# Kernel tuning notes

Measured on AMD Instinct MI355X. Metric: run time of the kernel, lower is better.

Reference implementation:

```python
import jax, jax.numpy as jnp
import numpy as np

NMS_THR = 0.7
TOPK = 128      # fixed post-NMS rois per level (static padding for jit)
OUT = 14        # RoIAlign output size
SAMPLES = 2     # samples per bin per dim (fixed approximation of sampling_ratio=-1)
STRIDES = (32.0, 16.0, 8.0)


def get_channel(a):
    # a: [..., 4] boxes as (cx, cy, w, h); FPN level assignment, clamped to [1, 4]
    s = jnp.sqrt(a[..., 2] * a[..., 3])
    return jnp.clip(jnp.floor(3.0 + jnp.log2(s / 224.0)), 1.0, 4.0)


def cxcywh_to_xyxy(b):
    cx, cy, w, h = b[..., 0], b[..., 1], b[..., 2], b[..., 3]
    return jnp.stack([cx - w / 2, cy - h / 2, cx + w / 2, cy + h / 2], axis=-1)


def pairwise_iou(b):
    x1, y1, x2, y2 = b[:, 0], b[:, 1], b[:, 2], b[:, 3]
    area = jnp.maximum(x2 - x1, 0.0) * jnp.maximum(y2 - y1, 0.0)
    ix1 = jnp.maximum(x1[:, None], x1[None, :])
    iy1 = jnp.maximum(y1[:, None], y1[None, :])
    ix2 = jnp.minimum(x2[:, None], x2[None, :])
    iy2 = jnp.minimum(y2[:, None], y2[None, :])
    inter = jnp.maximum(ix2 - ix1, 0.0) * jnp.maximum(iy2 - iy1, 0.0)
    union = area[:, None] + area[None, :] - inter
    return inter / jnp.maximum(union, 1e-9)


def nms_keep(boxes_xyxy, scores, thr):
    # Greedy NMS over masked scores (-inf entries sort last and are excluded later).
    n = scores.shape[0]
    order = jnp.argsort(-scores)
    iou = pairwise_iou(boxes_xyxy[order])  # [N, N]
    idx = jnp.arange(n)

    def body(sup, i):
        keep_i = ~sup[i]
        sup = sup | (keep_i & (iou[i] > thr) & (idx > i))
        return sup, keep_i

    _, keeps_sorted = jax.lax.scan(body, jnp.zeros(n, dtype=bool), idx)
    return jnp.zeros(n, dtype=bool).at[order].set(keeps_sorted)


def roi_align(feat, boxes):
    # feat: [C, H, W]; boxes: [K, 4]. NOTE: the original prepare_boxes feeds
    # (cx, cy, w, h) straight into RoIAlign, which interprets them as
    # (x1, y1, x2, y2) -- replicated faithfully here. spatial_scale = 1.
    C, H, W = feat.shape
    K = boxes.shape[0]
    x1, y1, x2, y2 = boxes[:, 0], boxes[:, 1], boxes[:, 2], boxes[:, 3]
    rw = jnp.maximum(x2 - x1, 1.0)
    rh = jnp.maximum(y2 - y1, 1.0)
    bw = rw / OUT
    bh = rh / OUT
    # fractional bin offsets, [OUT*SAMPLES]
    f = (jnp.arange(OUT, dtype=feat.dtype)[:, None]
         + (jnp.arange(SAMPLES, dtype=feat.dtype)[None, :] + 0.5) / SAMPLES).reshape(-1)
    ys = y1[:, None] + bh[:, None] * f[None, :]  # [K, S]
    xs = x1[:, None] + bw[:, None] * f[None, :]
    Y = ys[:, :, None]  # [K, S, 1]
    X = xs[:, None, :]  # [K, 1, S]
    valid = (Y > -1.0) & (Y < H) & (X > -1.0) & (X < W)  # [K, S, S]
    Yc = jnp.clip(Y, 0.0, H - 1.0)
    Xc = jnp.clip(X, 0.0, W - 1.0)
    y0 = jnp.floor(Yc)
    x0 = jnp.floor(Xc)
    y0i = y0.astype(jnp.int32)
    x0i = x0.astype(jnp.int32)
    y1i = jnp.minimum(y0i + 1, H - 1)
    x1i = jnp.minimum(x0i + 1, W - 1)
    ly = Yc - y0
    lx = Xc - x0
    hy = 1.0 - ly
    hx = 1.0 - lx
    g = lambda yi, xi: feat[:, yi, xi]  # -> [C, K, S, S]
    val = (g(y0i, x0i) * (hy * hx) + g(y0i, x1i) * (hy * lx)
           + g(y1i, x0i) * (ly * hx) + g(y1i, x1i) * (ly * lx))
    val = val * valid.astype(val.dtype)
    val = val.reshape(C, K, OUT, SAMPLES, OUT, SAMPLES).mean(axis=(3, 5))
    return jnp.transpose(val, (1, 0, 2, 3))  # [K, C, OUT, OUT]


def level_extract(feat, boxes, scores, levs, nl):
    # one image, one target FPN level: mask, NMS, fixed top-K select, RoIAlign
    mask = levs == nl
    msc = jnp.where(mask, scores, -jnp.inf)
    xyxy = cxcywh_to_xyxy(boxes)
    keep = nms_keep(jax.lax.stop_gradient(xyxy), jax.lax.stop_gradient(msc), NMS_THR)
    eff = jnp.where(keep & mask, msc, -jnp.inf)
    vals, sel = jax.lax.top_k(jax.lax.stop_gradient(eff), TOPK)
    valid = jnp.isfinite(vals)
    rois = boxes[sel] * valid[:, None].astype(boxes.dtype)
    out = roi_align(feat, rois)
    return out * valid[:, None, None, None].astype(out.dtype)


def _forward(p32, p16, p8, p4, a32, a16, a8, s32, s16, s8):
    anchors = (a32, a16, a8)  # p4 proposals are computed then discarded in the
    # original (grouping loop only runs l in range(3)); p4 features are never
    # RoIAligned either (nl loops 1..3), so p4 only appears as an unused input.
    levs = jnp.concatenate([get_channel(a) for a in anchors], axis=1)      # [B, N]
    boxes = jnp.concatenate([a * s for a, s in zip(anchors, STRIDES)], axis=1)
    scores = jnp.concatenate([s32, s16, s8], axis=1)
    outs = []
    for nl, feat in zip((1.0, 2.0, 3.0), (p32, p16, p8)):
        fn = jax.vmap(lambda f, b, s, l, nl=nl: level_extract(f, b, s, l, nl))
        outs.append(fn(feat, boxes, scores, levs))  # [B, TOPK, C, 14, 14]
    return jnp.concatenate(outs, axis=1)  # [B, 3*TOPK, C, 14, 14]


def setup_inputs():
    key = jax.random.key(0)
    ks = jax.random.split(key, 10)
    B, C = 2, 256
    p32 = jax.random.normal(ks[0], (B, C, 32, 32), jnp.float32)
    p16 = jax.random.normal(ks[1], (B, C, 64, 64), jnp.float32)
    p8 = jax.random.normal(ks[2], (B, C, 128, 128), jnp.float32)
    p4 = jax.random.normal(ks[3], (B, C, 256, 256), jnp.float32)

    def mk_anchors(k, n, hf):
        k1, k2 = jax.random.split(k)
        cxy = jax.random.uniform(k1, (B, n, 2), jnp.float32) * hf
        wh = 16.0 + jax.random.uniform(k2, (B, n, 2), jnp.float32) * 434.0
        return jnp.concatenate([cxy, wh], axis=-1)

    anchors_32 = mk_anchors(ks[4], 512, 32.0)
    anchors_16 = mk_anchors(ks[5], 1024, 64.0)
    anchors_8 = mk_anchors(ks[6], 2048, 128.0)
    scores_32 = jax.random.normal(ks[7], (B, 512), jnp.float32)
    scores_16 = jax.random.normal(ks[8], (B, 1024), jnp.float32)
    scores_8 = jax.random.normal(ks[9], (B, 2048), jnp.float32)
    return dict(p32=p32, p16=p16, p8=p8, p4=p4,
                anchors_32=anchors_32, anchors_16=anchors_16, anchors_8=anchors_8,
                scores_32=scores_32, scores_16=scores_16, scores_8=scores_8)


def reference(p32, p16, p8, p4, anchors_32, anchors_16, anchors_8,
              scores_32, scores_16, scores_8):
    return _forward(p32, p16, p8, p4, anchors_32, anchors_16, anchors_8,
                    scores_32, scores_16, scores_8)
```

## Files before the change

kernel.cpp:

```cpp
#include <hip/hip_runtime.h>
#include <stdint.h>

#define NMS_THR 0.7f
#define TOPK 128
#define NTOT 3584
#define NROW 4096
#define NW 64
#define OUTSZ 14
#define NSAMP 28

typedef unsigned long long u64;
typedef float vf4 __attribute__((ext_vector_type(4)));

__device__ __forceinline__ void fetch_anchor(
    const float* __restrict__ a32, const float* __restrict__ a16,
    const float* __restrict__ a8,
    const float* __restrict__ s32, const float* __restrict__ s16,
    const float* __restrict__ s8,
    int b, int i, float* A, float* st, float* sc)
{
    const float* P;
    if (i < 512) {
        P = a32 + (b * 512 + i) * 4;  *st = 32.0f; *sc = s32[b * 512 + i];
    } else if (i < 1536) {
        int j = i - 512;
        P = a16 + (b * 1024 + j) * 4; *st = 16.0f; *sc = s16[b * 1024 + j];
    } else {
        int j = i - 1536;
        P = a8 + (b * 2048 + j) * 4;  *st = 8.0f;  *sc = s8[b * 2048 + j];
    }
    A[0] = P[0]; A[1] = P[1]; A[2] = P[2]; A[3] = P[3];
}

__global__ __launch_bounds__(1024) void sortprep_kernel(
    const float* __restrict__ a32, const float* __restrict__ a16,
    const float* __restrict__ a8,
    const float* __restrict__ s32, const float* __restrict__ s16,
    const float* __restrict__ s8,
    float* __restrict__ sbox,
    float* __restrict__ scbox,
    int* __restrict__ mArr)
{
    __shared__ u64 key[NROW];
    __shared__ int mCount;
    int prob = blockIdx.x;
    int b = prob / 3;
    int nl = prob % 3 + 1;
    int tid = threadIdx.x;

    if (tid == 0) mCount = 0;
    __syncthreads();

    for (int i = tid; i < NTOT; i += 1024) {
        float A[4], st, sc;
        fetch_anchor(a32, a16, a8, s32, s16, s8, b, i, A, &st, &sc);
        float s = sqrtf(__fmul_rn(A[2], A[3]));
        float lv = floorf(__fadd_rn(3.0f, log2f(__fdiv_rn(s, 224.0f))));
        lv = fminf(fmaxf(lv, 1.0f), 4.0f);
        if ((int)lv == nl) {
            unsigned u = __float_as_uint(sc);
            u = (u & 0x80000000u) ? ~u : (u | 0x80000000u);
            unsigned d = ~u;
            int pos = atomicAdd(&mCount, 1);
            key[pos] = ((u64)d << 32) | (unsigned)i;
        }
    }
    __syncthreads();
    int m = mCount;
    int P2 = 64;
    while (P2 < m) P2 <<= 1;
    for (int i = m + tid; i < P2; i += 1024) key[i] = ~0ull;
    __syncthreads();

    for (int k = 2; k <= P2; k <<= 1) {
        for (int j = k >> 1; j > 0; j >>= 1) {
            for (int t = tid; t < P2; t += 1024) {
                int ixj = t ^ j;
                if (ixj > t) {
                    u64 a = key[t], bb = key[ixj];
                    bool up = ((t & k) == 0);
                    if ((a > bb) == up) { key[t] = bb; key[ixj] = a; }
                }
            }
            __syncthreads();
        }
    }

    for (int r = tid; r < m; r += 1024) {
        int orig = (int)(key[r] & 0xffffffffu);
        float A[4], st, sc;
        fetch_anchor(a32, a16, a8, s32, s16, s8, b, orig, A, &st, &sc);
        float cx = A[0] * st, cy = A[1] * st, w = A[2] * st, h = A[3] * st;
        float4 cw = make_float4(cx, cy, w, h);
        float4 v;
        v.x = __fsub_rn(cx, 0.5f * w);
        v.y = __fsub_rn(cy, 0.5f * h);
        v.z = __fadd_rn(cx, 0.5f * w);
        v.w = __fadd_rn(cy, 0.5f * h);
        ((float4*)(sbox + (size_t)prob * NROW * 4))[r] = v;
        ((float4*)(scbox + (size_t)prob * NROW * 4))[r] = cw;
    }
    if (tid == 0) mArr[prob] = m;
}

__global__ __launch_bounds__(256) void mask_kernel(
    const float* __restrict__ sbox, const int* __restrict__ mArr,
    u64* __restrict__ mask)
{
    int prob = blockIdx.x >> 10;
    int rgrp = blockIdx.x & 1023;
    int wave = threadIdx.x >> 6;
    int lane = threadIdx.x & 63;
    int row = rgrp * 4 + wave;
    int m = mArr[prob];
    if (row >= m) return;

    const float4* SB = (const float4*)(sbox + (size_t)prob * NROW * 4);
    float4 bi = SB[row];
    float areai = __fmul_rn(fmaxf(__fsub_rn(bi.z, bi.x), 0.0f),
                            fmaxf(__fsub_rn(bi.w, bi.y), 0.0f));
    u64* outm = mask + ((size_t)prob * NROW + row) * NW;
    int cEnd = (m - 1) >> 6;
    for (int c = row >> 6; c <= cEnd; c++) {
        int col = c * 64 + lane;
        bool p = false;
        if (col < m) {
            float4 bj = SB[col];
            float areaj = __fmul_rn(fmaxf(__fsub_rn(bj.z, bj.x), 0.0f),
                                    fmaxf(__fsub_rn(bj.w, bj.y), 0.0f));
            float ix1 = fmaxf(bi.x, bj.x);
            float iy1 = fmaxf(bi.y, bj.y);
            float ix2 = fminf(bi.z, bj.z);
            float iy2 = fminf(bi.w, bj.w);
            float inter = __fmul_rn(fmaxf(__fsub_rn(ix2, ix1), 0.0f),
                                    fmaxf(__fsub_rn(iy2, iy1), 0.0f));
            float uni = __fsub_rn(__fadd_rn(areai, areaj), inter);
            float iou = __fdiv_rn(inter, fmaxf(uni, 1e-9f));
            p = iou > NMS_THR;
        }
        u64 bal = __ballot(p);
        if (lane == 0) outm[c] = bal;
    }
}

__global__ __launch_bounds__(64) void scan_kernel(
    const float* __restrict__ scbox, const int* __restrict__ mArr,
    const u64* __restrict__ mask,
    float* __restrict__ rois,
    int* __restrict__ validOut)
{
    __shared__ int selList[TOPK];
    int prob = blockIdx.x;
    int lane = threadIdx.x;
    int m = mArr[prob];
    const u64* M = mask + (size_t)prob * NROW * NW;

    u64 sup;
    if (lane * 64 >= m) sup = ~0ull;
    else if (lane * 64 + 64 > m) sup = ~0ull << (m & 63);
    else sup = 0ull;

    int kept = 0;
    int cur = 0;
    while (kept < TOPK && cur < m) {
        int cw = cur >> 6;
        u64 validm = (lane < cw) ? 0ull : (lane == cw ? (~0ull << (cur & 63)) : ~0ull);
        u64 avail = ~sup & validm;
        u64 bal = __ballot(avail != 0ull);
        if (bal == 0ull) break;
        int fl = __builtin_ctzll(bal);
        int lo = __shfl((int)(unsigned)avail, fl);
        int hi = __shfl((int)(avail >> 32), fl);
        u64 w = ((u64)(unsigned)hi << 32) | (unsigned)lo;
        int j = fl * 64 + __builtin_ctzll(w);

        if (lane == 0) selList[kept] = j;
        kept++;
        if (lane >= (j >> 6)) sup |= M[(size_t)j * NW + lane];
        cur = j + 1;
    }
    __syncthreads();

    for (int k = lane; k < TOPK; k += 64) {
        float4 rv = make_float4(0.0f, 0.0f, 0.0f, 0.0f);
        int vld = 0;
        if (k < kept) {
            rv = ((const float4*)(scbox + (size_t)prob * NROW * 4))[selList[k]];
            vld = 1;
        }
        ((float4*)(rois + ((size_t)prob * TOPK + k) * 4))[0] = rv;
        validOut[prob * TOPK + k] = vld;
    }
}

__global__ __launch_bounds__(256) void repack_kernel(
    const float* __restrict__ p32, const float* __restrict__ p16,
    const float* __restrict__ p8,
    float* __restrict__ ft0, float* __restrict__ ft1, float* __restrict__ ft2)
{
    __shared__ float tile[64][65];
    int id = blockIdx.x;
    const float* F; float* T; int HW, b, t;
    if (id < 128)       { F = p32; T = ft0; HW = 1024;  b = id / 64;  t = id % 64; }
    else if (id < 640)  { id -= 128; F = p16; T = ft1; HW = 4096;  b = id / 256; t = id % 256; }
    else                { id -= 640; F = p8;  T = ft2; HW = 16384; b = id / 1024; t = id % 1024; }
    int hw0 = (t >> 2) * 64;
    int c0 = (t & 3) * 64;
    int tid = threadIdx.x;
    int lane16 = tid & 15;
    int grp16 = tid >> 4;

    for (int i = 0; i < 4; i++) {
        int c_l = i * 16 + grp16;
        int hw_l = lane16 * 4;
        vf4 v = *(const vf4*)(F + ((size_t)b * 256 + c0 + c_l) * HW + hw0 + hw_l);
        tile[c_l][hw_l + 0] = v.x;
        tile[c_l][hw_l + 1] = v.y;
        tile[c_l][hw_l + 2] = v.z;
        tile[c_l][hw_l + 3] = v.w;
    }
    __syncthreads();
    for (int i = 0; i < 4; i++) {
        int hw_l = i * 16 + grp16;
        int c_l = lane16 * 4;
        vf4 v;
        v.x = tile[c_l + 0][hw_l];
        v.y = tile[c_l + 1][hw_l];
        v.z = tile[c_l + 2][hw_l];
        v.w = tile[c_l + 3][hw_l];
        *(vf4*)(T + ((size_t)b * HW + hw0 + hw_l) * 256 + c0 + c_l) = v;
    }
}

__global__ __launch_bounds__(256) void zerofill_kernel(vf4* __restrict__ out, int n4)
{
    vf4 z = (vf4)0.0f;
    int stride = gridDim.x * 256;
    for (int i = blockIdx.x * 256 + threadIdx.x; i < n4; i += stride)
        out[i] = z;
}

__global__ __launch_bounds__(256) void roialign_kernel(
    const float* __restrict__ ft0, const float* __restrict__ ft1,
    const float* __restrict__ ft2,
    const float* __restrict__ rois, const int* __restrict__ validIn,
    float* __restrict__ out)
{
    int roiIdx = blockIdx.x;
    int b = roiIdx / 384;
    int slot = roiIdx - b * 384;
    int lvl = slot / TOPK;
    int k = slot - lvl * TOPK;
    int prob = b * 3 + lvl;

    int vld = validIn[prob * TOPK + k];
    if (!vld) return;

    int W;
    const float* ft;
    if (lvl == 0)      { W = 32;  ft = ft0; }
    else if (lvl == 1) { W = 64;  ft = ft1; }
    else               { W = 128; ft = ft2; }
    int HW = W * W;
    const vf4* F4 = (const vf4*)(ft + (size_t)b * HW * 256);
    float* O = out + (size_t)roiIdx * 256 * 196;
    int tid = threadIdx.x;

    __shared__ int sx0[NSAMP], sx1[NSAMP], sy0[NSAMP], sy1[NSAMP];
    __shared__ float shx[NSAMP], slx[NSAMP], shy[NSAMP], sly[NSAMP];
    __shared__ int sxv[NSAMP], syv[NSAMP];
    __shared__ int oiL[OUTSZ], ojL[OUTSZ];
    __shared__ int nyx[2];

    if (tid < 2 * NSAMP) {
        const float* R = rois + ((size_t)prob * TOPK + k) * 4;
        float x1 = R[0], y1 = R[1], x2 = R[2], y2 = R[3];
        float rw = fmaxf(__fsub_rn(x2, x1), 1.0f);
        float rh = fmaxf(__fsub_rn(y2, y1), 1.0f);
        float bw = __fdiv_rn(rw, 14.0f);
        float bh = __fdiv_rn(rh, 14.0f);
        int axis = tid / NSAMP;
        int s = tid - axis * NSAMP;
        float fi = (float)(s >> 1) + ((s & 1) ? 0.75f : 0.25f);
        float start = axis ? y1 : x1;
        float bsz = axis ? bh : bw;
        float lim = (float)W;
        float X = __fadd_rn(start, __fmul_rn(bsz, fi));
        bool v = (X > -1.0f) && (X < lim);
        float Xc = fminf(fmaxf(X, 0.0f), lim - 1.0f);
        float x0f = floorf(Xc);
        int x0 = (int)x0f;
        int xp1 = min(x0 + 1, W - 1);
        float l = __fsub_rn(Xc, x0f);
        float hh = __fsub_rn(1.0f, l);
        float vf = v ? 1.0f : 0.0f;
        if (axis == 0) { sx0[s] = x0; sx1[s] = xp1; shx[s] = hh * vf; slx[s] = l * vf; sxv[s] = v ? 1 : 0; }
        else           { sy0[s] = x0; sy1[s] = xp1; shy[s] = hh * vf; sly[s] = l * vf; syv[s] = v ? 1 : 0; }
    }
    __syncthreads();

    if (tid == 0) {
        int n = 0;
        for (int oi = 0; oi < OUTSZ; oi++)
            if (syv[2 * oi] | syv[2 * oi + 1]) oiL[n++] = oi;
        nyx[0] = n;
    }
    if (tid == 1) {
        int n = 0;
        for (int oj = 0; oj < OUTSZ; oj++)
            if (sxv[2 * oj] | sxv[2 * oj + 1]) ojL[n++] = oj;
        nyx[1] = n;
    }
    __syncthreads();

    int ny = nyx[0], nx = nyx[1];
    int total = ny * nx;
    if (total == 0) return;

    int w = tid >> 6;
    int lane = tid & 63;

    for (int ci = w; ci < total; ci += 4) {
        int oi = oiL[ci / nx];
        int oj = ojL[ci - (ci / nx) * nx];
        int sA = oi * 2, sB = sA + 1;
        int tA = oj * 2, tB = tA + 1;
        int y0A = sy0[sA], y1A = sy1[sA], y0B = sy0[sB], y1B = sy1[sB];
        int x0A = sx0[tA], x1A = sx1[tA], x0B = sx0[tB], x1B = sx1[tB];
        float hyA = shy[sA], lyA = sly[sA], hyB = shy[sB], lyB = sly[sB];
        float hxA = shx[tA], lxA = slx[tA], hxB = shx[tB], lxB = slx[tB];

        #define TAP(Y, X) F4[((Y) * W + (X)) * 64 + lane]
        vf4 a00 = TAP(y0A, x0A), a01 = TAP(y0A, x1A);
        vf4 a10 = TAP(y1A, x0A), a11 = TAP(y1A, x1A);
        vf4 b00 = TAP(y0A, x0B), b01 = TAP(y0A, x1B);
        vf4 b10 = TAP(y1A, x0B), b11 = TAP(y1A, x1B);
        vf4 c00 = TAP(y0B, x0A), c01 = TAP(y0B, x1A);
        vf4 c10 = TAP(y1B, x0A), c11 = TAP(y1B, x1A);
        vf4 d00 = TAP(y0B, x0B), d01 = TAP(y0B, x1B);
        vf4 d10 = TAP(y1B, x0B), d11 = TAP(y1B, x1B);
        #undef TAP

        vf4 s00 = hyA * (hxA * a00 + lxA * a01) + lyA * (hxA * a10 + lxA * a11);
        vf4 s01 = hyA * (hxB * b00 + lxB * b01) + lyA * (hxB * b10 + lxB * b11);
        vf4 s10 = hyB * (hxA * c00 + lxA * c01) + lyB * (hxA * c10 + lxA * c11);
        vf4 s11 = hyB * (hxB * d00 + lxB * d01) + lyB * (hxB * d10 + lxB * d11);
        vf4 acc = 0.25f * (s00 + s01 + s10 + s11);

        int p = oi * 14 + oj;
        O[(4 * lane + 0) * 196 + p] = acc.x;
        O[(4 * lane + 1) * 196 + p] = acc.y;
        O[(4 * lane + 2) * 196 + p] = acc.z;
        O[(4 * lane + 3) * 196 + p] = acc.w;
    }
}

extern "C" void kernel_launch(void* const* d_in, const int* in_sizes, int n_in,
                              void* d_out, int out_size, void* d_ws, size_t ws_size,
                              hipStream_t stream) {
    const float* p32 = (const float*)d_in[0];
    const float* p16 = (const float*)d_in[1];
    const float* p8  = (const float*)d_in[2];
    const float* a32 = (const float*)d_in[4];
    const float* a16 = (const float*)d_in[5];
    const float* a8  = (const float*)d_in[6];
    const float* s32 = (const float*)d_in[7];
    const float* s16 = (const float*)d_in[8];
    const float* s8  = (const float*)d_in[9];
    float* out = (float*)d_out;

    const size_t offValid = 3072;
    const size_t offMArr  = offValid + 768;
    const size_t offSbox  = offMArr + 8;
    const size_t offScbox = offSbox + (size_t)6 * NROW * 4;
    const size_t offMask  = offScbox + (size_t)6 * NROW * 4;
    const size_t offFt    = offMask + (size_t)6 * NROW * NW * 2;
    const size_t totalFloats = offFt + 11010048;

    float* base;
    if (ws_size >= totalFloats * 4) {
        base = (float*)d_ws;
    } else {
        base = (float*)d_in[3];
    }
    float* rois  = base;
    int*   valid = (int*)(base + offValid);
    int*   mArr  = (int*)(base + offMArr);
    float* sbox  = base + offSbox;
    float* scbox = base + offScbox;
    u64*   maskb = (u64*)(base + offMask);
    float* ft0   = base + offFt;
    float* ft1   = ft0 + 524288;
    float* ft2   = ft1 + 2097152;

    zerofill_kernel<<<2048, 256, 0, stream>>>((vf4*)out, out_size / 4);
    sortprep_kernel<<<6, 1024, 0, stream>>>(a32, a16, a8, s32, s16, s8,
                                            sbox, scbox, mArr);
    mask_kernel<<<6 * 1024, 256, 0, stream>>>(sbox, mArr, maskb);
    scan_kernel<<<6, 64, 0, stream>>>(scbox, mArr, maskb, rois, valid);
    repack_kernel<<<2688, 256, 0, stream>>>(p32, p16, p8, ft0, ft1, ft2);
    roialign_kernel<<<768, 256, 0, stream>>>(ft0, ft1, ft2, rois, valid, out);
}
```

Measured before the change: 410.6 us.

## Drop NHWC repack and sample NCHW features directly; fuse zerofill into mask kernel

Removes the transpose kernel that copied the feature maps into a channel-last workspace. RoIAlign now reads the original channel-first maps using paired float2 loads along x, with clamped base indices so both taps stay in bounds. The output zero-fill moves into the IoU mask kernel, which saves two launches and avoids writing and rereading the repacked features. The trade-off is that gathers across channels are now strided by HW per lane and no longer coalesced, which may hurt RoIAlign memory efficiency.

```diff
diff --git a/kernel.cpp b/kernel.cpp
--- a/kernel.cpp
+++ b/kernel.cpp
@@ -11,6 +11,7 @@
 
 typedef unsigned long long u64;
 typedef float vf4 __attribute__((ext_vector_type(4)));
+typedef float float2u __attribute__((ext_vector_type(2), aligned(4)));
 
 __device__ __forceinline__ void fetch_anchor(
     const float* __restrict__ a32, const float* __restrict__ a16,
@@ -103,9 +104,10 @@
     if (tid == 0) mArr[prob] = m;
 }
 
-__global__ __launch_bounds__(256) void mask_kernel(
+__global__ __launch_bounds__(256) void maskfill_kernel(
     const float* __restrict__ sbox, const int* __restrict__ mArr,
-    u64* __restrict__ mask)
+    u64* __restrict__ mask,
+    vf4* __restrict__ out, int n4)
 {
     int prob = blockIdx.x >> 10;
     int rgrp = blockIdx.x & 1023;
@@ -113,34 +115,40 @@
     int lane = threadIdx.x & 63;
     int row = rgrp * 4 + wave;
     int m = mArr[prob];
-    if (row >= m) return;
-
-    const float4* SB = (const float4*)(sbox + (size_t)prob * NROW * 4);
-    float4 bi = SB[row];
-    float areai = __fmul_rn(fmaxf(__fsub_rn(bi.z, bi.x), 0.0f),
-                            fmaxf(__fsub_rn(bi.w, bi.y), 0.0f));
-    u64* outm = mask + ((size_t)prob * NROW + row) * NW;
-    int cEnd = (m - 1) >> 6;
-    for (int c = row >> 6; c <= cEnd; c++) {
-        int col = c * 64 + lane;
-        bool p = false;
-        if (col < m) {
-            float4 bj = SB[col];
-            float areaj = __fmul_rn(fmaxf(__fsub_rn(bj.z, bj.x), 0.0f),
-                                    fmaxf(__fsub_rn(bj.w, bj.y), 0.0f));
-            float ix1 = fmaxf(bi.x, bj.x);
-            float iy1 = fmaxf(bi.y, bj.y);
-            float ix2 = fminf(bi.z, bj.z);
-            float iy2 = fminf(bi.w, bj.w);
-            float inter = __fmul_rn(fmaxf(__fsub_rn(ix2, ix1), 0.0f),
-                                    fmaxf(__fsub_rn(iy2, iy1), 0.0f));
-            float uni = __fsub_rn(__fadd_rn(areai, areaj), inter);
-            float iou = __fdiv_rn(inter, fmaxf(uni, 1e-9f));
-            p = iou > NMS_THR;
-        }
-        u64 bal = __ballot(p);
-        if (lane == 0) outm[c] = bal;
-    }
+
+    if (row < m) {
+        const float4* SB = (const float4*)(sbox + (size_t)prob * NROW * 4);
+        float4 bi = SB[row];
+        float areai = __fmul_rn(fmaxf(__fsub_rn(bi.z, bi.x), 0.0f),
+                                fmaxf(__fsub_rn(bi.w, bi.y), 0.0f));
+        u64* outm = mask + ((size_t)prob * NROW + row) * NW;
+        int cEnd = (m - 1) >> 6;
+        for (int c = row >> 6; c <= cEnd; c++) {
+            int col = c * 64 + lane;
+            bool p = false;
+            if (col < m) {
+                float4 bj = SB[col];
+                float areaj = __fmul_rn(fmaxf(__fsub_rn(bj.z, bj.x), 0.0f),
+                                        fmaxf(__fsub_rn(bj.w, bj.y), 0.0f));
+                float ix1 = fmaxf(bi.x, bj.x);
+                float iy1 = fmaxf(bi.y, bj.y);
+                float ix2 = fminf(bi.z, bj.z);
+                float iy2 = fminf(bi.w, bj.w);
+                float inter = __fmul_rn(fmaxf(__fsub_rn(ix2, ix1), 0.0f),
+                                        fmaxf(__fsub_rn(iy2, iy1), 0.0f));
+                float uni = __fsub_rn(__fadd_rn(areai, areaj), inter);
+                float iou = __fdiv_rn(inter, fmaxf(uni, 1e-9f));
+                p = iou > NMS_THR;
+            }
+            u64 bal = __ballot(p);
+            if (lane == 0) outm[c] = bal;
+        }
+    }
+
+    vf4 z = (vf4)0.0f;
+    int stride = gridDim.x * 256;
+    for (int i = blockIdx.x * 256 + threadIdx.x; i < n4; i += stride)
+        out[i] = z;
 }
 
 __global__ __launch_bounds__(64) void scan_kernel(
@@ -193,56 +201,9 @@
     }
 }
 
-__global__ __launch_bounds__(256) void repack_kernel(
+__global__ __launch_bounds__(256) void roialign_kernel(
     const float* __restrict__ p32, const float* __restrict__ p16,
     const float* __restrict__ p8,
-    float* __restrict__ ft0, float* __restrict__ ft1, float* __restrict__ ft2)
-{
-    __shared__ float tile[64][65];
-    int id = blockIdx.x;
-    const float* F; float* T; int HW, b, t;
-    if (id < 128)       { F = p32; T = ft0; HW = 1024;  b = id / 64;  t = id % 64; }
-    else if (id < 640)  { id -= 128; F = p16; T = ft1; HW = 4096;  b = id / 256; t = id % 256; }
-    else                { id -= 640; F = p8;  T = ft2; HW = 16384; b = id / 1024; t = id % 1024; }
-    int hw0 = (t >> 2) * 64;
-    int c0 = (t & 3) * 64;
-    int tid = threadIdx.x;
-    int lane16 = tid & 15;
-    int grp16 = tid >> 4;
-
-    for (int i = 0; i < 4; i++) {
-        int c_l = i * 16 + grp16;
-        int hw_l = lane16 * 4;
-        vf4 v = *(const vf4*)(F + ((size_t)b * 256 + c0 + c_l) * HW + hw0 + hw_l);
-        tile[c_l][hw_l + 0] = v.x;
-        tile[c_l][hw_l + 1] = v.y;
-        tile[c_l][hw_l + 2] = v.z;
-        tile[c_l][hw_l + 3] = v.w;
-    }
-    __syncthreads();
-    for (int i = 0; i < 4; i++) {
-        int hw_l = i * 16 + grp16;
-        int c_l = lane16 * 4;
-        vf4 v;
-        v.x = tile[c_l + 0][hw_l];
-        v.y = tile[c_l + 1][hw_l];
-        v.z = tile[c_l + 2][hw_l];
-        v.w = tile[c_l + 3][hw_l];
-        *(vf4*)(T + ((size_t)b * HW + hw0 + hw_l) * 256 + c0 + c_l) = v;
-    }
-}
-
-__global__ __launch_bounds__(256) void zerofill_kernel(vf4* __restrict__ out, int n4)
-{
-    vf4 z = (vf4)0.0f;
-    int stride = gridDim.x * 256;
-    for (int i = blockIdx.x * 256 + threadIdx.x; i < n4; i += stride)
-        out[i] = z;
-}
-
-__global__ __launch_bounds__(256) void roialign_kernel(
-    const float* __restrict__ ft0, const float* __restrict__ ft1,
-    const float* __restrict__ ft2,
     const float* __restrict__ rois, const int* __restrict__ validIn,
     float* __restrict__ out)
 {
@@ -257,17 +218,17 @@
     if (!vld) return;
 
     int W;
-    const float* ft;
-    if (lvl == 0)      { W = 32;  ft = ft0; }
-    else if (lvl == 1) { W = 64;  ft = ft1; }
-    else               { W = 128; ft = ft2; }
+    const float* feat;
+    if (lvl == 0)      { W = 32;  feat = p32; }
+    else if (lvl == 1) { W = 64;  feat = p16; }
+    else               { W = 128; feat = p8; }
     int HW = W * W;
-    const vf4* F4 = (const vf4*)(ft + (size_t)b * HW * 256);
+    const float* F0 = feat + (size_t)b * 256 * HW;
     float* O = out + (size_t)roiIdx * 256 * 196;
     int tid = threadIdx.x;
 
-    __shared__ int sx0[NSAMP], sx1[NSAMP], sy0[NSAMP], sy1[NSAMP];
-    __shared__ float shx[NSAMP], slx[NSAMP], shy[NSAMP], sly[NSAMP];
+    __shared__ int sxb[NSAMP], sy0[NSAMP], sy1[NSAMP];
+    __shared__ float swx0[NSAMP], swx1[NSAMP], shy[NSAMP], sly[NSAMP];
     __shared__ int sxv[NSAMP], syv[NSAMP];
     __shared__ int oiL[OUTSZ], ojL[OUTSZ];
     __shared__ int nyx[2];
@@ -290,12 +251,18 @@
         float Xc = fminf(fmaxf(X, 0.0f), lim - 1.0f);
         float x0f = floorf(Xc);
         int x0 = (int)x0f;
-        int xp1 = min(x0 + 1, W - 1);
         float l = __fsub_rn(Xc, x0f);
         float hh = __fsub_rn(1.0f, l);
         float vf = v ? 1.0f : 0.0f;
-        if (axis == 0) { sx0[s] = x0; sx1[s] = xp1; shx[s] = hh * vf; slx[s] = l * vf; sxv[s] = v ? 1 : 0; }
-        else           { sy0[s] = x0; sy1[s] = xp1; shy[s] = hh * vf; sly[s] = l * vf; syv[s] = v ? 1 : 0; }
+        if (axis == 0) {
+            int base; float w0, w1;
+            if (x0 >= W - 1) { base = W - 2; w0 = 0.0f; w1 = vf; }
+            else             { base = x0;    w0 = hh * vf; w1 = l * vf; }
+            sxb[s] = base; swx0[s] = w0; swx1[s] = w1; sxv[s] = v ? 1 : 0;
+        } else {
+            sy0[s] = x0; sy1[s] = min(x0 + 1, W - 1);
+            shy[s] = hh * vf; sly[s] = l * vf; syv[s] = v ? 1 : 0;
+        }
     }
     __syncthreads();
 
@@ -326,32 +293,35 @@
         int sA = oi * 2, sB = sA + 1;
         int tA = oj * 2, tB = tA + 1;
         int y0A = sy0[sA], y1A = sy1[sA], y0B = sy0[sB], y1B = sy1[sB];
-        int x0A = sx0[tA], x1A = sx1[tA], x0B = sx0[tB], x1B = sx1[tB];
         float hyA = shy[sA], lyA = sly[sA], hyB = shy[sB], lyB = sly[sB];
-        float hxA = shx[tA], lxA = slx[tA], hxB = shx[tB], lxB = slx[tB];
-
-        #define TAP(Y, X) F4[((Y) * W + (X)) * 64 + lane]
-        vf4 a00 = TAP(y0A, x0A), a01 = TAP(y0A, x1A);
-        vf4 a10 = TAP(y1A, x0A), a11 = TAP(y1A, x1A);
-        vf4 b00 = TAP(y0A, x0B), b01 = TAP(y0A, x1B);
-        vf4 b10 = TAP(y1A, x0B), b11 = TAP(y1A, x1B);
-        vf4 c00 = TAP(y0B, x0A), c01 = TAP(y0B, x1A);
-        vf4 c10 = TAP(y1B, x0A), c11 = TAP(y1B, x1A);
-        vf4 d00 = TAP(y0B, x0B), d01 = TAP(y0B, x1B);
-        vf4 d10 = TAP(y1B, x0B), d11 = TAP(y1B, x1B);
-        #undef TAP
-
-        vf4 s00 = hyA * (hxA * a00 + lxA * a01) + lyA * (hxA * a10 + lxA * a11);
-        vf4 s01 = hyA * (hxB * b00 + lxB * b01) + lyA * (hxB * b10 + lxB * b11);
-        vf4 s10 = hyB * (hxA * c00 + lxA * c01) + lyB * (hxA * c10 + lxA * c11);
-        vf4 s11 = hyB * (hxB * d00 + lxB * d01) + lyB * (hxB * d10 + lxB * d11);
-        vf4 acc = 0.25f * (s00 + s01 + s10 + s11);
-
+        int xA = sxb[tA], xB = sxb[tB];
+        float xw0A = swx0[tA], xw1A = swx1[tA];
+        float xw0B = swx0[tB], xw1B = swx1[tB];
         int p = oi * 14 + oj;
-        O[(4 * lane + 0) * 196 + p] = acc.x;
-        O[(4 * lane + 1) * 196 + p] = acc.y;
-        O[(4 * lane + 2) * 196 + p] = acc.z;
-        O[(4 * lane + 3) * 196 + p] = acc.w;
+
+        for (int it = 0; it < 4; it++) {
+            int c = lane + it * 64;
+            const float* F = F0 + c * HW;
+            const float* rA0 = F + y0A * W;
+            const float* rA1 = F + y1A * W;
+            const float* rB0 = F + y0B * W;
+            const float* rB1 = F + y1B * W;
+
+            float2u a0 = *(const float2u*)(rA0 + xA);
+            float2u a1 = *(const float2u*)(rA1 + xA);
+            float2u c0 = *(const float2u*)(rA0 + xB);
+            float2u c1 = *(const float2u*)(rA1 + xB);
+            float2u b0 = *(const float2u*)(rB0 + xA);
+            float2u b1 = *(const float2u*)(rB1 + xA);
+            float2u d0 = *(const float2u*)(rB0 + xB);
+            float2u d1 = *(const float2u*)(rB1 + xB);
+
+            float s00 = hyA * (xw0A * a0.x + xw1A * a0.y) + lyA * (xw0A * a1.x + xw1A * a1.y);
+            float s01 = hyA * (xw0B * c0.x + xw1B * c0.y) + lyA * (xw0B * c1.x + xw1B * c1.y);
+            float s10 = hyB * (xw0A * b0.x + xw1A * b0.y) + lyB * (xw0A * b1.x + xw1A * b1.y);
+            float s11 = hyB * (xw0B * d0.x + xw1B * d0.y) + lyB * (xw0B * d1.x + xw1B * d1.y);
+            O[c * 196 + p] = 0.25f * (s00 + s01 + s10 + s11);
+        }
     }
 }
 
@@ -374,8 +344,7 @@
     const size_t offSbox  = offMArr + 8;
     const size_t offScbox = offSbox + (size_t)6 * NROW * 4;
     const size_t offMask  = offScbox + (size_t)6 * NROW * 4;
-    const size_t offFt    = offMask + (size_t)6 * NROW * NW * 2;
-    const size_t totalFloats = offFt + 11010048;
+    const size_t totalFloats = offMask + (size_t)6 * NROW * NW * 2;
 
     float* base;
     if (ws_size >= totalFloats * 4) {
@@ -389,15 +358,11 @@
     float* sbox  = base + offSbox;
     float* scbox = base + offScbox;
     u64*   maskb = (u64*)(base + offMask);
-    float* ft0   = base + offFt;
-    float* ft1   = ft0 + 524288;
-    float* ft2   = ft1 + 2097152;
-
-    zerofill_kernel<<<2048, 256, 0, stream>>>((vf4*)out, out_size / 4);
+
     sortprep_kernel<<<6, 1024, 0, stream>>>(a32, a16, a8, s32, s16, s8,
                                             sbox, scbox, mArr);
-    mask_kernel<<<6 * 1024, 256, 0, stream>>>(sbox, mArr, maskb);
+    maskfill_kernel<<<6 * 1024, 256, 0, stream>>>(sbox, mArr, maskb,
+                                                  (vf4*)out, out_size / 4);
     scan_kernel<<<6, 64, 0, stream>>>(scbox, mArr, maskb, rois, valid);
-    repack_kernel<<<2688, 256, 0, stream>>>(p32, p16, p8, ft0, ft1, ft2);
-    roialign_kernel<<<768, 256, 0, stream>>>(ft0, ft1, ft2, rois, valid, out);
-}
+    roialign_kernel<<<768, 256, 0, stream>>>(p32, p16, p8, rois, valid, out);
+}
```

Result: faster. 374.4 us (-8.8%).
